# Kernel tuning notes

Hardware: AMD Instinct MI355X
Metric: run time of the kernel (lower is better)

The kernel has to match this reference:

```python
import jax, jax.numpy as jnp
import numpy as np
from jax import lax

B_SZ, C_IN, C_OUT, H_IM, W_IM = 2, 128, 128, 64, 64
N_STATE = 16
DT_RANK = 4  # ceil(128/32)


def _ln_cf(x, w, b, eps=1e-6):
    # channels_first LayerNorm over channel dim
    u = x.mean(1, keepdims=True)
    s = ((x - u) ** 2).mean(1, keepdims=True)
    return w[None, :, None, None] * (x - u) / jnp.sqrt(s + eps) + b[None, :, None, None]


def _bn_train(x, g, b, eps=1e-5):
    # BatchNorm2d in training mode (batch statistics, biased variance)
    m = x.mean((0, 2, 3), keepdims=True)
    v = ((x - m) ** 2).mean((0, 2, 3), keepdims=True)
    return g[None, :, None, None] * (x - m) / jnp.sqrt(v + eps) + b[None, :, None, None]


def _dwconv(x, w, b):
    y = lax.conv_general_dilated(x, w, (1, 1), 'SAME', feature_group_count=x.shape[1],
                                 dimension_numbers=('NCHW', 'OIHW', 'NCHW'))
    return y + b[None, :, None, None]


def _conv1x1(x, w, b):
    return jnp.einsum('oi,bihw->bohw', w, x) + b[None, :, None, None]


def _selective_scan(u, dt, A, Bm, Cm, D, delta_bias):
    # u, dt: [B,Ch,L]; A: [Ch,N]; Bm, Cm: [B,N,L]; D: [Ch]
    dt = jax.nn.softplus(dt + delta_bias[None, :, None])
    xs = (dt.transpose(2, 0, 1), u.transpose(2, 0, 1), Bm.transpose(2, 0, 1), Cm.transpose(2, 0, 1))
    h0 = jnp.zeros(u.shape[:2] + (A.shape[1],), u.dtype)

    def step(h, inp):
        dt_t, u_t, b_t, c_t = inp
        dA = jnp.exp(dt_t[..., None] * A)                        # [B,Ch,N]
        h = h * dA + (dt_t * u_t)[..., None] * b_t[:, None, :]   # [B,Ch,N]
        return h, jnp.einsum('bcn,bn->bc', h, c_t)

    _, ys = lax.scan(step, h0, xs)
    return ys.transpose(1, 2, 0) + u * D[None, :, None]


def _ssm_apply(u, Wx, bx, Wdt, bdt, Alog, D, r):
    # u: [B,Ch,L]. Replicates torch row-major .reshape of [(B L),D] -> [B,D,L].
    Bb, Ch, L = u.shape
    N = Alog.shape[1]
    x_flat = u.transpose(0, 2, 1).reshape(Bb * L, Ch)   # 'b c l -> (b l) c'
    x_dbl = x_flat @ Wx.T + bx
    dt = (x_dbl[:, :r] @ Wdt.T + bdt).reshape(Bb, Wdt.shape[0], L)
    Bm = x_dbl[:, r:r + N].reshape(Bb, N, L)
    Cm = x_dbl[:, r + N:].reshape(Bb, N, L)
    return _selective_scan(u, dt, -jnp.exp(Alog), Bm, Cm, D, bdt)


def _forward(x, ln_in_w, ln_in_b, inproj_w, inproj_b, ln_mamba_w, ln_mamba_b, convm_w, convm_b,
             convr_w, convr_b, ln_cat_w, ln_cat_b, xproj_f_w, xproj_f_b, dtproj_f_w, dtproj_f_b,
             Alog_f, D_f, xproj_b_w, xproj_b_b, dtproj_b_w, dtproj_b_b, Alog_b, D_b,
             xproj_u_w, xproj_u_b, dtproj_u_w, dtproj_u_b, Alog_u, D_u, gate1_w, gate1_b,
             bn_g, bn_b, gate2_w, gate2_b, outproj_w, outproj_b, outln_w, outln_b):
    Bb, C, H, W = x.shape
    L = H * W
    half = C // 2
    x = _ln_cf(x, ln_in_w, ln_in_b)
    xp = _conv1x1(x, inproj_w, inproj_b)
    x_mamba, x_res = xp[:, :C], xp[:, C:]
    x_mamba = _ln_cf(x_mamba, ln_mamba_w, ln_mamba_b)
    x_mamba = jax.nn.silu(_dwconv(x_mamba, convm_w, convm_b))
    x_res = jax.nn.silu(_dwconv(x_res, convr_w, convr_b))
    # forward scan on first half of channels
    xf = x_mamba[:, :half].reshape(Bb, half, L)
    yf = _ssm_apply(xf, xproj_f_w, xproj_f_b, dtproj_f_w, dtproj_f_b, Alog_f, D_f, DT_RANK).reshape(Bb, half, H, W)
    # backward scan on second half (flip H,W, scan, flip back)
    xb = x_mamba[:, half:][:, :, ::-1, ::-1]
    yb = _ssm_apply(xb.reshape(Bb, half, L), xproj_b_w, xproj_b_b, dtproj_b_w, dtproj_b_b,
                    Alog_b, D_b, DT_RANK).reshape(Bb, half, H, W)[:, :, ::-1, ::-1]
    concat = _ln_cf(jnp.concatenate([yf, yb], axis=1), ln_cat_w, ln_cat_b)
    # uncertainty-ordered scan on full x_mamba
    sig = jax.nn.sigmoid(x_mamba.mean(1, keepdims=True))
    unc = (-(sig * jnp.log(sig + 1e-6))).reshape(Bb, L)
    idx = jnp.argsort(-unc, axis=1)       # descending uncertainty
    inv = jnp.argsort(idx, axis=1)        # inverse permutation
    xs = jnp.take_along_axis(x_mamba.reshape(Bb, C, L), idx[:, None, :], axis=2)
    yu = _ssm_apply(xs, xproj_u_w, xproj_u_b, dtproj_u_w, dtproj_u_b, Alog_u, D_u, 2 * DT_RANK)
    yu = jnp.take_along_axis(yu, inv[:, None, :], axis=2).reshape(Bb, C, H, W)
    # gated fusion
    g = jax.nn.relu(_bn_train(_conv1x1(jnp.concatenate([concat, yu], 1), gate1_w, gate1_b), bn_g, bn_b))
    g = jax.nn.sigmoid(_conv1x1(g, gate2_w, gate2_b))
    fused = g * yu + (1.0 - g) * concat
    out = _conv1x1(jnp.concatenate([fused, x_res], 1), outproj_w, outproj_b)
    return _ln_cf(out, outln_w, outln_b)


def setup_inputs() -> dict:
    key = jax.random.key(0)
    ks = jax.random.split(key, 16)
    C, half, R, N = C_IN, C_IN // 2, DT_RANK, N_STATE
    rn = lambda k, shp, s=0.02: jax.random.normal(k, shp, jnp.float32) * s

    def inv_dt(k, n):
        dt = jnp.exp(jax.random.uniform(k, (n,)) * (np.log(0.1) - np.log(0.001)) + np.log(0.001))
        dt = jnp.maximum(dt, 1e-4)
        return dt + jnp.log(-jnp.expm1(-dt))

    std = R ** -0.5
    Alog_h = jnp.log(jnp.broadcast_to(jnp.arange(1, N + 1, dtype=jnp.float32), (half, N)))
    Alog_fl = jnp.log(jnp.broadcast_to(jnp.arange(1, N + 1, dtype=jnp.float32), (C, N)))
    return {
        'x': jax.random.normal(ks[0], (B_SZ, C, H_IM, W_IM), jnp.float32),
        'ln_in_w': jnp.ones(C), 'ln_in_b': jnp.zeros(C),
        'inproj_w': rn(ks[1], (2 * C, C)), 'inproj_b': jnp.zeros(2 * C),
        'ln_mamba_w': jnp.ones(C), 'ln_mamba_b': jnp.zeros(C),
        'convm_w': rn(ks[2], (C, 1, 3, 3), 0.1), 'convm_b': jnp.zeros(C),
        'convr_w': rn(ks[3], (C, 1, 3, 3), 0.1), 'convr_b': jnp.zeros(C),
        'ln_cat_w': jnp.ones(C), 'ln_cat_b': jnp.zeros(C),
        'xproj_f_w': rn(ks[4], (R + 2 * N, half)), 'xproj_f_b': jnp.zeros(R + 2 * N),
        'dtproj_f_w': jax.random.uniform(ks[5], (half, R), minval=-std, maxval=std),
        'dtproj_f_b': inv_dt(ks[6], half),
        'Alog_f': Alog_h, 'D_f': jnp.ones(half),
        'xproj_b_w': rn(ks[7], (R + 2 * N, half)), 'xproj_b_b': jnp.zeros(R + 2 * N),
        'dtproj_b_w': jax.random.uniform(ks[8], (half, R), minval=-std, maxval=std),
        'dtproj_b_b': inv_dt(ks[9], half),
        'Alog_b': Alog_h, 'D_b': jnp.ones(half),
        'xproj_u_w': rn(ks[10], (2 * R + 2 * N, C)), 'xproj_u_b': jnp.zeros(2 * R + 2 * N),
        'dtproj_u_w': jax.random.uniform(ks[11], (C, 2 * R), minval=-std, maxval=std),
        'dtproj_u_b': inv_dt(ks[12], C),
        'Alog_u': Alog_fl, 'D_u': jnp.ones(C),
        'gate1_w': rn(ks[13], (C, 2 * C)), 'gate1_b': jnp.zeros(C),
        'bn_g': jnp.ones(C), 'bn_b': jnp.zeros(C),
        'gate2_w': rn(ks[14], (C, C)), 'gate2_b': jnp.zeros(C),
        'outproj_w': rn(ks[15], (C_OUT, 2 * C)), 'outproj_b': jnp.zeros(C_OUT),
        'outln_w': jnp.ones(C_OUT), 'outln_b': jnp.zeros(C_OUT),
    }


def reference(x, ln_in_w, ln_in_b, inproj_w, inproj_b, ln_mamba_w, ln_mamba_b, convm_w, convm_b,
              convr_w, convr_b, ln_cat_w, ln_cat_b, xproj_f_w, xproj_f_b, dtproj_f_w, dtproj_f_b,
              Alog_f, D_f, xproj_b_w, xproj_b_b, dtproj_b_w, dtproj_b_b, Alog_b, D_b,
              xproj_u_w, xproj_u_b, dtproj_u_w, dtproj_u_b, Alog_u, D_u, gate1_w, gate1_b,
              bn_g, bn_b, gate2_w, gate2_b, outproj_w, outproj_b, outln_w, outln_b):
    return _forward(x, ln_in_w, ln_in_b, inproj_w, inproj_b, ln_mamba_w, ln_mamba_b, convm_w, convm_b,
                    convr_w, convr_b, ln_cat_w, ln_cat_b, xproj_f_w, xproj_f_b, dtproj_f_w, dtproj_f_b,
                    Alog_f, D_f, xproj_b_w, xproj_b_b, dtproj_b_w, dtproj_b_b, Alog_b, D_b,
                    xproj_u_w, xproj_u_b, dtproj_u_w, dtproj_u_b, Alog_u, D_u, gate1_w, gate1_b,
                    bn_g, bn_b, gate2_w, gate2_b, outproj_w, outproj_b, outln_w, outln_b)
```

## Files before the change

kernel.cpp:

```cpp
#include <hip/hip_runtime.h>
#include <cstdint>
#include <cstddef>

#define TPB 256

namespace {

constexpr int B_SZ = 2;
constexpr int C    = 128;
constexpr int HALF = 64;
constexpr int L    = 4096;
constexpr int N    = 16;
constexpr int HH   = 64;
constexpr int WW   = 64;

__device__ __forceinline__ float softplusf(float x) {
  return fmaxf(x, 0.f) + __logf(1.f + __expf(-fabsf(x)));
}
__device__ __forceinline__ float sigm(float x) { return 1.f / (1.f + __expf(-x)); }

__device__ __forceinline__ unsigned long long unc_key(float u, int i) {
  unsigned m = __float_as_uint(u);
  m = (m & 0x80000000u) ? ~m : (m | 0x80000000u);
  return ((unsigned long long)(~m) << 32) | (unsigned)i;
}

__global__ void k_conv_ln(const float* __restrict__ X, int bsX,
                          const float* __restrict__ lnw, const float* __restrict__ lnb,
                          const float* __restrict__ W, const float* __restrict__ bias,
                          float* __restrict__ Y, int I, int O,
                          float* __restrict__ st1s, float* __restrict__ st1q) {
  constexpr int O_PB = 8;
  __shared__ float Wl[O_PB * 128];
  __shared__ float aw[128], ab[128];
  const int o0 = blockIdx.y * O_PB;
  const int b  = blockIdx.z;
  for (int t = threadIdx.x; t < O_PB * I; t += TPB) {
    int i = t / O_PB, k = t % O_PB;
    Wl[t] = W[(size_t)(o0 + k) * I + i];
  }
  for (int t = threadIdx.x; t < I; t += TPB) { aw[t] = lnw[t]; ab[t] = lnb[t]; }
  __syncthreads();
  const int l0 = blockIdx.x * (2 * TPB) + threadIdx.x;
  const int l1 = l0 + TPB;
  const float* X0 = X + (size_t)b * bsX + l0;
  const float* X1 = X + (size_t)b * bsX + l1;
  float s0 = 0.f, q0 = 0.f, s1 = 0.f, q1 = 0.f;
#pragma unroll 8
  for (int i = 0; i < I; ++i) {
    float v0 = X0[(size_t)i * L], v1 = X1[(size_t)i * L];
    s0 += v0; q0 += v0 * v0; s1 += v1; q1 += v1 * v1;
  }
  const float m0 = s0 / I, m1 = s1 / I;
  const float r0 = rsqrtf(q0 / I - m0 * m0 + 1e-6f);
  const float r1 = rsqrtf(q1 / I - m1 * m1 + 1e-6f);
  float acc0[O_PB], acc1[O_PB];
#pragma unroll
  for (int k = 0; k < O_PB; ++k) { acc0[k] = bias[o0 + k]; acc1[k] = acc0[k]; }
#pragma unroll 4
  for (int i = 0; i < I; ++i) {
    float xv0 = (X0[(size_t)i * L] - m0) * r0 * aw[i] + ab[i];
    float xv1 = (X1[(size_t)i * L] - m1) * r1 * aw[i] + ab[i];
#pragma unroll
    for (int k = 0; k < O_PB; ++k) {
      acc0[k] += Wl[i * O_PB + k] * xv0;
      acc1[k] += Wl[i * O_PB + k] * xv1;
    }
  }
#pragma unroll
  for (int k = 0; k < O_PB; ++k) {
    Y[((size_t)b * O + o0 + k) * L + l0] = acc0[k];
    Y[((size_t)b * O + o0 + k) * L + l1] = acc1[k];
  }
  if (o0 < 128) {
    float ss0 = 0.f, qq0 = 0.f, ss1 = 0.f, qq1 = 0.f;
#pragma unroll
    for (int k = 0; k < O_PB; ++k) {
      ss0 += acc0[k]; qq0 += acc0[k] * acc0[k];
      ss1 += acc1[k]; qq1 += acc1[k] * acc1[k];
    }
    atomicAdd(&st1s[b * L + l0], ss0);
    atomicAdd(&st1q[b * L + l0], qq0);
    atomicAdd(&st1s[b * L + l1], ss1);
    atomicAdd(&st1q[b * L + l1], qq1);
  }
}

__global__ void k_dwconv_t(const float* __restrict__ xp,
                           const float* __restrict__ st1s, const float* __restrict__ st1q,
                           const float* __restrict__ lnw, const float* __restrict__ lnb,
                           const float* __restrict__ Wm, const float* __restrict__ bm,
                           const float* __restrict__ Wr, const float* __restrict__ br,
                           float* __restrict__ xm, float* __restrict__ xr) {
  const int c = blockIdx.y;
  const int z = blockIdx.z;
  const int b = z & 1, mode = z >> 1;
  const int h0 = blockIdx.x * 4;
  __shared__ float T[6][66];
  const float* Xc = xp + ((size_t)b * 2 * C + (mode ? C + c : c)) * L;
  const float lw = mode ? 0.f : lnw[c];
  const float lb2 = mode ? 0.f : lnb[c];
  for (int t = threadIdx.x; t < 6 * 66; t += TPB) {
    int r = t / 66, cc = t % 66 - 1;
    int hh = h0 - 1 + r;
    float v = 0.f;
    if (hh >= 0 && hh < HH && cc >= 0 && cc < WW) {
      int li = hh * WW + cc;
      v = Xc[li];
      if (mode == 0) {
        float sv = st1s[b * L + li], qv = st1q[b * L + li];
        float m = sv * (1.f / 128.f);
        float rr = rsqrtf(qv * (1.f / 128.f) - m * m + 1e-6f);
        v = (v - m) * rr * lw + lb2;
      }
    }
    T[r][t % 66] = v;
  }
  __syncthreads();
  const int hl = threadIdx.x >> 6, w = threadIdx.x & 63;
  const float* W9 = (mode ? Wr : Wm) + c * 9;
  float acc = mode ? br[c] : bm[c];
#pragma unroll
  for (int kh = 0; kh < 3; ++kh)
#pragma unroll
    for (int kw = 0; kw < 3; ++kw)
      acc += T[hl + kh][w + kw] * W9[kh * 3 + kw];
  const int l = (h0 + hl) * WW + w;
  float* Yp = mode ? xr : xm;
  Yp[((size_t)b * C + c) * L + l] = acc * sigm(acc);
}

__global__ void k_unc(const float* __restrict__ xm, float* __restrict__ unc) {
  const int lp = threadIdx.x & 63;
  const int wv = threadIdx.x >> 6;
  const int p  = blockIdx.x * 64 + lp;
  const int b = p / L, l = p % L;
  const float* Xp = xm + (size_t)b * C * L + l;
  float s = 0.f;
#pragma unroll 8
  for (int i = 0; i < 32; ++i) s += Xp[(size_t)(wv * 32 + i) * L];
  __shared__ float r1[4][64];
  r1[wv][lp] = s;
  __syncthreads();
  if (wv == 0) {
    float st = r1[0][lp] + r1[1][lp] + r1[2][lp] + r1[3][lp];
    float sg = sigm(st / C);
    unc[p] = -(sg * __logf(sg + 1e-6f));
  }
}

__global__ void k_rank(const float* __restrict__ unc, int* __restrict__ rankbuf) {
  constexpr int JC = 512;
  __shared__ unsigned long long K[JC];
  const int b  = blockIdx.z;
  const int j0 = blockIdx.y * JC;
  const int i  = blockIdx.x * TPB + threadIdx.x;
  for (int t = threadIdx.x; t < JC; t += TPB)
    K[t] = unc_key(unc[b * L + j0 + t], j0 + t);
  __syncthreads();
  const unsigned long long my = unc_key(unc[b * L + i], i);
  int cnt = 0;
#pragma unroll 8
  for (int j = 0; j < JC; ++j) cnt += (K[j] < my) ? 1 : 0;
  atomicAdd(&rankbuf[b * L + i], cnt);
}

__global__ void k_scatgath(const float* __restrict__ xm, const int* __restrict__ rankbuf,
                           float* __restrict__ xs, int* __restrict__ inv,
                           int* __restrict__ idx) {
  int t = blockIdx.x * TPB + threadIdx.x;
  int l = t % L, c = (t / L) % C, b = t / (C * L);
  int r = rankbuf[b * L + l];
  xs[((size_t)b * C + c) * L + r] = xm[t];
  if (c == 0) { inv[b * L + l] = r; idx[b * L + r] = l; }
}

__global__ void k_convx_all(const float* __restrict__ xm, const float* __restrict__ xs,
                            const float* __restrict__ Wf, const float* __restrict__ bf,
                            const float* __restrict__ Wb, const float* __restrict__ bb,
                            const float* __restrict__ Wu, const float* __restrict__ bu,
                            float* __restrict__ XDF, float* __restrict__ XDU) {
  const int z = blockIdx.z;
  const bool isU = z >= 4;
  const int I = isU ? 128 : 64;
  const int O = isU ? 40 : 36;
  const int o0 = blockIdx.y * 4;
  if (o0 >= O) return;
  int b, dir;
  const float *W, *bi;
  if (!isU) { dir = z >> 1; b = z & 1; W = dir ? Wb : Wf; bi = dir ? bb : bf; }
  else      { dir = 0; b = z - 4; W = Wu; bi = bu; }
  __shared__ float Wl[4 * 128];
  for (int t = threadIdx.x; t < 4 * I; t += TPB) {
    int i = t / 4, k = t % 4;
    Wl[t] = W[(size_t)(o0 + k) * I + i];
  }
  __syncthreads();
  const int l = blockIdx.x * TPB + threadIdx.x;
  const int ls = isU ? l : (dir ? (L - 1 - l) : l);
  const float* Xb = isU ? (xs + (size_t)b * C * L)
                        : (xm + ((size_t)b * C + dir * HALF) * L);
  float acc[4];
#pragma unroll
  for (int k = 0; k < 4; ++k) acc[k] = bi[o0 + k];
#pragma unroll 4
  for (int i = 0; i < I; ++i) {
    float xv = Xb[(size_t)i * L + ls];
#pragma unroll
    for (int k = 0; k < 4; ++k) acc[k] += Wl[i * 4 + k] * xv;
  }
  float* yp = isU ? (XDU + ((size_t)b * L + l) * 40 + o0)
                  : (XDF + ((size_t)z * L + l) * 36 + o0);
#pragma unroll
  for (int k = 0; k < 4; ++k) yp[k] = acc[k];
}

__global__ void k_bc_all(const float* __restrict__ xdblF, const float* __restrict__ xdblU,
                         float* __restrict__ BmTF, float* __restrict__ CmTF,
                         float* __restrict__ BmTU, float* __restrict__ CmTU) {
  const int z = blockIdx.z;
  const bool isU = z >= 4;
  const int RT = isU ? 8 : 4, OT = isU ? 40 : 36;
  const float* src = isU ? (xdblU + (size_t)(z - 4) * L * 40)
                         : (xdblF + (size_t)z * L * 36);
  float* BT = isU ? (BmTU + (size_t)(z - 4) * L * N) : (BmTF + (size_t)z * L * N);
  float* CT = isU ? (CmTU + (size_t)(z - 4) * L * N) : (CmTF + (size_t)z * L * N);
  const int n = blockIdx.y;
  const int l2 = blockIdx.x * TPB + threadIdx.x;
  int f2 = n * L + l2;
  int lb = f2 >> 4, cb = f2 & 15;
  const float* xr2 = src + (size_t)lb * OT + RT + cb;
  size_t ob = (size_t)l2 * N + n;
  BT[ob] = xr2[0];
  CT[ob] = xr2[N];
}

__global__ __launch_bounds__(1024) void
k_scan_all(const float* __restrict__ xdblF, const float* __restrict__ xdblU,
           const float* __restrict__ dtf_w, const float* __restrict__ dtf_b,
           const float* __restrict__ dtb_w, const float* __restrict__ dtb_b,
           const float* __restrict__ dtu_w, const float* __restrict__ dtu_b,
           const float* __restrict__ xm, const float* __restrict__ xs,
           const int* __restrict__ idx,
           const float* __restrict__ BmTF, const float* __restrict__ CmTF,
           const float* __restrict__ BmTU, const float* __restrict__ CmTU,
           const float* __restrict__ Alog_f, const float* __restrict__ Alog_b,
           const float* __restrict__ Alog_u,
           const float* __restrict__ D_f, const float* __restrict__ D_b,
           const float* __restrict__ D_u,
           float* __restrict__ yf, float* __restrict__ yb, float* __restrict__ yu) {
  const int blk = blockIdx.x;
  const int tid = threadIdx.x;
  const bool isU = blk >= 256;
  int CsT, RT, c, b, dir;
  const float *Wdt, *bdt, *Alog, *Dv, *xdbl, *BT, *CT, *Ub;
  const int* idxb = nullptr;
  float* Y;
  int OT;
  if (!isU) {
    CsT = 64; RT = 4; OT = 36;
    int zb = blk >> 6; c = blk & 63; dir = zb >> 1; b = zb & 1;
    Wdt = dir ? dtb_w : dtf_w; bdt = dir ? dtb_b : dtf_b;
    Alog = dir ? Alog_b : Alog_f; Dv = dir ? D_b : D_f;
    xdbl = xdblF + (size_t)zb * L * 36;
    BT = BmTF + (size_t)zb * L * N; CT = CmTF + (size_t)zb * L * N;
    Ub = xm + ((size_t)b * C + dir * HALF + c) * L;
    Y = (dir ? yb : yf) + ((size_t)b * HALF + c) * L;
  } else {
    CsT = 128; RT = 8; OT = 40;
    int blk2 = blk - 256; b = blk2 >> 7; c = blk2 & 127; dir = 0;
    Wdt = dtu_w; bdt = dtu_b; Alog = Alog_u; Dv = D_u;
    xdbl = xdblU + (size_t)b * L * 40;
    BT = BmTU + (size_t)b * L * N; CT = CmTU + (size_t)b * L * N;
    Ub = xs + ((size_t)b * C + c) * L;
    idxb = idx + b * L;
    Y = yu + ((size_t)b * C + c) * L;
  }
  __shared__ float sW[1024];
  __shared__ float sb2[128];
  __shared__ float dtL[64][65];
  __shared__ float uL[64][65];
  __shared__ float sA[N][65], sH[N][65];
  for (int t = tid; t < CsT * RT; t += 1024) {
    int csrc = t / RT, r = t % RT;
    sW[r * CsT + csrc] = Wdt[t];
  }
  for (int t = tid; t < CsT; t += 1024) sb2[t] = bdt[t];
  __syncthreads();
  {
    const int chunk_d = tid >> 4;
    const int sq = (tid & 15) * 4;
    const int lsrc = isU ? (c * 32 + (chunk_d >> 1)) : (c * 64 + chunk_d);
    const float* xrp = xdbl + (size_t)lsrc * OT;
    float xr[8];
    for (int r = 0; r < RT; ++r) xr[r] = xrp[r];
    const float bcc = sb2[c];
#pragma unroll
    for (int j = 0; j < 4; ++j) {
      int s = sq + j;
      int csrc = isU ? (((chunk_d & 1) << 6) + s) : s;
      float acc = sb2[csrc] + bcc;
      for (int r = 0; r < RT; ++r) acc += sW[r * CsT + csrc] * xr[r];
      int l = (chunk_d << 6) + s;
      dtL[chunk_d][s] = softplusf(acc);
      uL[chunk_d][s] = Ub[isU ? l : (dir ? (L - 1 - l) : l)];
    }
  }
  __syncthreads();
  const int n = tid & 15;
  const int chunk = tid >> 4;
  const float a = -__expf(Alog[c * N + n]);
  const float* bp = BT + ((size_t)(chunk << 6)) * N + n;
  const float* cp = CT + ((size_t)(chunk << 6)) * N + n;
  float ap = 1.f, h = 0.f;
#pragma unroll 4
  for (int s = 0; s < 64; ++s) {
    float d = dtL[chunk][s];
    float uv = uL[chunk][s];
    float bn = bp[(size_t)s * N];
    float dA = __expf(d * a);
    ap *= dA;
    h = h * dA + d * uv * bn;
  }
  sA[n][chunk] = ap; sH[n][chunk] = h;
  __syncthreads();
  {
    const int w = tid >> 6;
    const int k = tid & 63;
    float A = sA[w][k];
    float Bv = sH[w][k];
#pragma unroll
    for (int j = 1; j < 64; j <<= 1) {
      float pa = __shfl_up(A, j);
      float pb = __shfl_up(Bv, j);
      if (k >= j) { Bv = pb * A + Bv; A = pa * A; }
    }
    float hprev = __shfl_up(Bv, 1);
    sH[w][k] = (k == 0) ? 0.f : hprev;
  }
  __syncthreads();
  h = sH[n][chunk];
  const float Dc = Dv[c];
  float ybuf[4];
#pragma unroll 4
  for (int s = 0; s < 64; ++s) {
    float d = dtL[chunk][s];
    float uv = uL[chunk][s];
    float bn = bp[(size_t)s * N];
    float cn = cp[(size_t)s * N];
    float dA = __expf(d * a);
    h = h * dA + d * uv * bn;
    float p = h * cn;
    p += __shfl_xor(p, 1);
    p += __shfl_xor(p, 2);
    p += __shfl_xor(p, 4);
    p += __shfl_xor(p, 8);
    if ((s & 15) == n) ybuf[s >> 4] = p + uv * Dc;
  }
  if (!isU) {
    float* Yp = Y + (chunk << 6);
#pragma unroll
    for (int q = 0; q < 4; ++q) Yp[16 * q + n] = ybuf[q];
  } else {
    const int s0 = chunk << 6;
#pragma unroll
    for (int q = 0; q < 4; ++q) Y[idxb[s0 + 16 * q + n]] = ybuf[q];
  }
}

template <int O_PB>
__global__ void k_gate1(const float* __restrict__ yf, const float* __restrict__ yb,
                        const float* __restrict__ lncw, const float* __restrict__ lncb,
                        const float* __restrict__ yu,
                        const float* __restrict__ W, const float* __restrict__ bias,
                        float* __restrict__ g1,
                        float* __restrict__ st2m, float* __restrict__ st2r,
                        float* __restrict__ bnsum) {
  __shared__ float Wl[O_PB * 256];
  __shared__ float cw[128], cb2[128];
  __shared__ float part[2][O_PB][4];
  const int o0 = blockIdx.y * O_PB;
  const int b  = blockIdx.z;
  for (int t = threadIdx.x; t < O_PB * 256; t += TPB) {
    int i = t / O_PB, k = t % O_PB;
    Wl[t] = W[(size_t)(o0 + k) * 256 + i];
  }
  for (int t = threadIdx.x; t < 128; t += TPB) { cw[t] = lncw[t]; cb2[t] = lncb[t]; }
  __syncthreads();
  const int l = blockIdx.x * TPB + threadIdx.x;
  const float* f0 = yf + (size_t)b * HALF * L + l;
  const float* b0 = yb + (size_t)b * HALF * L + (L - 1 - l);
  const float* u0 = yu + (size_t)b * C * L + l;
  float s = 0.f, s2 = 0.f;
#pragma unroll 8
  for (int i = 0; i < 64; ++i) { float v = f0[(size_t)i * L]; s += v; s2 += v * v; }
#pragma unroll 8
  for (int i = 0; i < 64; ++i) { float v = b0[(size_t)i * L]; s += v; s2 += v * v; }
  const float m = s / C;
  const float r = rsqrtf(s2 / C - m * m + 1e-6f);
  if (blockIdx.y == 0) { st2m[b * L + l] = m; st2r[b * L + l] = r; }
  float acc[O_PB];
#pragma unroll
  for (int k = 0; k < O_PB; ++k) acc[k] = bias[o0 + k];
#pragma unroll 4
  for (int i = 0; i < 64; ++i) {
    float cv = (f0[(size_t)i * L] - m) * r * cw[i] + cb2[i];
#pragma unroll
    for (int k = 0; k < O_PB; ++k) acc[k] += Wl[i * O_PB + k] * cv;
  }
#pragma unroll 4
  for (int i = 0; i < 64; ++i) {
    float cv = (b0[(size_t)i * L] - m) * r * cw[64 + i] + cb2[64 + i];
#pragma unroll
    for (int k = 0; k < O_PB; ++k) acc[k] += Wl[(64 + i) * O_PB + k] * cv;
  }
#pragma unroll 4
  for (int i = 0; i < 128; ++i) {
    float xv = u0[(size_t)i * L];
#pragma unroll
    for (int k = 0; k < O_PB; ++k) acc[k] += Wl[(128 + i) * O_PB + k] * xv;
  }
#pragma unroll
  for (int k = 0; k < O_PB; ++k)
    g1[((size_t)b * C + o0 + k) * L + l] = acc[k];
  const int wv = threadIdx.x >> 6, lnn = threadIdx.x & 63;
#pragma unroll
  for (int k = 0; k < O_PB; ++k) {
    float v = acc[k];
    v += __shfl_xor(v, 1);  v += __shfl_xor(v, 2);  v += __shfl_xor(v, 4);
    v += __shfl_xor(v, 8);  v += __shfl_xor(v, 16); v += __shfl_xor(v, 32);
    if (lnn == 0) part[0][k][wv] = v;
    float q = acc[k] * acc[k];
    q += __shfl_xor(q, 1);  q += __shfl_xor(q, 2);  q += __shfl_xor(q, 4);
    q += __shfl_xor(q, 8);  q += __shfl_xor(q, 16); q += __shfl_xor(q, 32);
    if (lnn == 0) part[1][k][wv] = q;
  }
  __syncthreads();
  if (threadIdx.x < 2 * O_PB) {
    int which = threadIdx.x >= O_PB, k = threadIdx.x % O_PB;
    float v = part[which][k][0] + part[which][k][1] + part[which][k][2] + part[which][k][3];
    atomicAdd(&bnsum[which * 128 + o0 + k], v);
  }
}

template <int O_PB>
__global__ void k_gate2_fuse(const float* __restrict__ g1,
                             const float* __restrict__ bnsum,
                             const float* __restrict__ bn_g, const float* __restrict__ bn_b,
                             const float* __restrict__ W, const float* __restrict__ bias,
                             const float* __restrict__ yu,
                             const float* __restrict__ yf, const float* __restrict__ yb,
                             const float* __restrict__ mean2, const float* __restrict__ rinv2,
                             const float* __restrict__ lncw, const float* __restrict__ lncb,
                             float* __restrict__ fused) {
  __shared__ float Wl[O_PB * 128];
  __shared__ float sc[128], sh[128];
  __shared__ float cwo[O_PB], cbo[O_PB];
  const int o0 = blockIdx.y * O_PB;
  const int b  = blockIdx.z;
  for (int t = threadIdx.x; t < O_PB * 128; t += TPB) {
    int i = t / O_PB, k = t % O_PB;
    Wl[t] = W[(size_t)(o0 + k) * 128 + i];
  }
  for (int t = threadIdx.x; t < 128; t += TPB) {
    float sv = bnsum[t], qv = bnsum[128 + t];
    float mean = sv / (B_SZ * L);
    float var  = qv / (B_SZ * L) - mean * mean;
    float scv = bn_g[t] * rsqrtf(var + 1e-5f);
    sc[t] = scv;
    sh[t] = bn_b[t] - mean * scv;
  }
  if (threadIdx.x < O_PB) {
    cwo[threadIdx.x] = lncw[o0 + threadIdx.x];
    cbo[threadIdx.x] = lncb[o0 + threadIdx.x];
  }
  __syncthreads();
  const int l = blockIdx.x * TPB + threadIdx.x;
  const float m = mean2[b * L + l], r = rinv2[b * L + l];
  const float* Xb = g1 + (size_t)b * C * L + l;
  float acc[O_PB];
#pragma unroll
  for (int k = 0; k < O_PB; ++k) acc[k] = bias[o0 + k];
#pragma unroll 4
  for (int i = 0; i < 128; ++i) {
    float v = fmaxf(Xb[(size_t)i * L] * sc[i] + sh[i], 0.f);
#pragma unroll
    for (int k = 0; k < O_PB; ++k) acc[k] += Wl[i * O_PB + k] * v;
  }
#pragma unroll
  for (int k = 0; k < O_PB; ++k) {
    int o = o0 + k;
    float g = sigm(acc[k]);
    float yuv = yu[((size_t)b * C + o) * L + l];
    float yv = (o < 64) ? yf[((size_t)b * HALF + o) * L + l]
                        : yb[((size_t)b * HALF + (o - 64)) * L + (L - 1 - l)];
    float cv = (yv - m) * r * cwo[k] + cbo[k];
    fused[((size_t)b * C + o) * L + l] = g * yuv + (1.f - g) * cv;
  }
}

template <int O_PB>
__global__ void k_conv1x1_cat2(const float* __restrict__ X1, const float* __restrict__ X2,
                               const float* __restrict__ W, const float* __restrict__ bias,
                               float* __restrict__ Y, int O) {
  __shared__ float Wl[O_PB * 256];
  const int o0 = blockIdx.y * O_PB;
  const int b  = blockIdx.z;
  for (int t = threadIdx.x; t < O_PB * 256; t += TPB) {
    int i = t / O_PB, k = t % O_PB;
    Wl[t] = W[(size_t)(o0 + k) * 256 + i];
  }
  __syncthreads();
  const int l = blockIdx.x * TPB + threadIdx.x;
  const float* Xb1 = X1 + (size_t)b * C * L + l;
  const float* Xb2 = X2 + (size_t)b * C * L + l;
  float acc[O_PB];
#pragma unroll
  for (int k = 0; k < O_PB; ++k) acc[k] = bias[o0 + k];
#pragma unroll 4
  for (int i = 0; i < 128; ++i) {
    float xv = Xb1[(size_t)i * L];
#pragma unroll
    for (int k = 0; k < O_PB; ++k) acc[k] += Wl[i * O_PB + k] * xv;
  }
#pragma unroll 4
  for (int i = 0; i < 128; ++i) {
    float xv = Xb2[(size_t)i * L];
#pragma unroll
    for (int k = 0; k < O_PB; ++k) acc[k] += Wl[(128 + i) * O_PB + k] * xv;
  }
#pragma unroll
  for (int k = 0; k < O_PB; ++k)
    Y[((size_t)b * O + o0 + k) * L + l] = acc[k];
}

__global__ void k_ln_cf(const float* __restrict__ X,
                        const float* __restrict__ w, const float* __restrict__ bchan,
                        float* __restrict__ Y) {
  const int lp = threadIdx.x & 63;
  const int wv = threadIdx.x >> 6;
  const int p  = blockIdx.x * 64 + lp;
  const int b = p / L, l = p % L;
  const float* Xp = X + (size_t)b * C * L + l;
  float s = 0.f, s2 = 0.f;
#pragma unroll 8
  for (int i = 0; i < 32; ++i) {
    float v = Xp[(size_t)(wv * 32 + i) * L];
    s += v; s2 += v * v;
  }
  __shared__ float r1[4][64], r2[4][64];
  r1[wv][lp] = s; r2[wv][lp] = s2;
  __syncthreads();
  float st  = r1[0][lp] + r1[1][lp] + r1[2][lp] + r1[3][lp];
  float s2t = r2[0][lp] + r2[1][lp] + r2[2][lp] + r2[3][lp];
  float mean = st / C;
  float rinv = rsqrtf(s2t / C - mean * mean + 1e-6f);
  float* Yp = Y + (size_t)b * C * L + l;
#pragma unroll 8
  for (int i = 0; i < 32; ++i) {
    int c = wv * 32 + i;
    float v = Xp[(size_t)c * L];
    Yp[(size_t)c * L] = w[c] * (v - mean) * rinv + bchan[c];
  }
}

}

extern "C" void kernel_launch(void* const* d_in, const int* in_sizes, int n_in,
                              void* d_out, int out_size, void* d_ws, size_t ws_size,
                              hipStream_t stream) {
  const float* x         = (const float*)d_in[0];
  const float* ln_in_w   = (const float*)d_in[1];
  const float* ln_in_b   = (const float*)d_in[2];
  const float* inproj_w  = (const float*)d_in[3];
  const float* inproj_b  = (const float*)d_in[4];
  const float* ln_m_w    = (const float*)d_in[5];
  const float* ln_m_b    = (const float*)d_in[6];
  const float* convm_w   = (const float*)d_in[7];
  const float* convm_b   = (const float*)d_in[8];
  const float* convr_w   = (const float*)d_in[9];
  const float* convr_b   = (const float*)d_in[10];
  const float* ln_cat_w  = (const float*)d_in[11];
  const float* ln_cat_b  = (const float*)d_in[12];
  const float* xpf_w     = (const float*)d_in[13];
  const float* xpf_b     = (const float*)d_in[14];
  const float* dtf_w     = (const float*)d_in[15];
  const float* dtf_b     = (const float*)d_in[16];
  const float* Alog_f    = (const float*)d_in[17];
  const float* D_f       = (const float*)d_in[18];
  const float* xpb_w     = (const float*)d_in[19];
  const float* xpb_b     = (const float*)d_in[20];
  const float* dtb_w     = (const float*)d_in[21];
  const float* dtb_b     = (const float*)d_in[22];
  const float* Alog_b    = (const float*)d_in[23];
  const float* D_b       = (const float*)d_in[24];
  const float* xpu_w     = (const float*)d_in[25];
  const float* xpu_b     = (const float*)d_in[26];
  const float* dtu_w     = (const float*)d_in[27];
  const float* dtu_b     = (const float*)d_in[28];
  const float* Alog_u    = (const float*)d_in[29];
  const float* D_u       = (const float*)d_in[30];
  const float* gate1_w   = (const float*)d_in[31];
  const float* gate1_b   = (const float*)d_in[32];
  const float* bn_g      = (const float*)d_in[33];
  const float* bn_b      = (const float*)d_in[34];
  const float* gate2_w   = (const float*)d_in[35];
  const float* gate2_b   = (const float*)d_in[36];
  const float* outproj_w = (const float*)d_in[37];
  const float* outproj_b = (const float*)d_in[38];
  const float* outln_w   = (const float*)d_in[39];
  const float* outln_b   = (const float*)d_in[40];

  float* ws = (float*)d_ws;
  size_t off = 0;
  auto alloc = [&](size_t n) { float* p = ws + off; off += n; return p; };

  const size_t BL = (size_t)B_SZ * L;
  float* st1s  = alloc(BL);
  float* st1q  = alloc(BL);
  int*   rank  = (int*)alloc(BL);
  float* bnsum = alloc(256);
  const size_t zeroBytes = (3 * BL + 256) * sizeof(float);

  float* xp    = alloc((size_t)B_SZ * 2 * C * L);
  float* xm    = alloc((size_t)B_SZ * C * L);
  float* xr    = alloc((size_t)B_SZ * C * L);
  float* unc   = alloc(BL);
  int*   inv   = (int*)alloc(BL);
  int*   idx   = (int*)alloc(BL);
  float* xs    = alloc((size_t)B_SZ * C * L);
  float* xdblF = alloc((size_t)4 * L * 36);
  float* BmTF  = alloc((size_t)4 * L * N);
  float* CmTF  = alloc((size_t)4 * L * N);
  float* xdblU = alloc((size_t)2 * L * 40);
  float* BmTU  = alloc((size_t)2 * L * N);
  float* CmTU  = alloc((size_t)2 * L * N);
  float* yf    = alloc((size_t)B_SZ * HALF * L);
  float* yb    = alloc((size_t)B_SZ * HALF * L);
  float* yu    = alloc((size_t)B_SZ * C * L);
  float* st2m  = alloc(BL);
  float* st2r  = alloc(BL);
  float* g1    = alloc((size_t)B_SZ * C * L);
  float* fused = alloc((size_t)B_SZ * C * L);
  float* outp  = alloc((size_t)B_SZ * C * L);
  (void)ws_size; (void)in_sizes; (void)n_in; (void)out_size;

  const int pixB = B_SZ * L / 64;
  const int elemB = B_SZ * C * L / TPB;

  hipMemsetAsync(st1s, 0, zeroBytes, stream);
  k_conv_ln<<<dim3(L / (2 * TPB), 32, B_SZ), TPB, 0, stream>>>(
      x, C * L, ln_in_w, ln_in_b, inproj_w, inproj_b, xp, 128, 256, st1s, st1q);
  k_dwconv_t<<<dim3(HH / 4, C, 2 * B_SZ), TPB, 0, stream>>>(
      xp, st1s, st1q, ln_m_w, ln_m_b, convm_w, convm_b, convr_w, convr_b, xm, xr);
  k_unc<<<pixB, TPB, 0, stream>>>(xm, unc);
  k_rank<<<dim3(L / TPB, 8, B_SZ), TPB, 0, stream>>>(unc, rank);
  k_scatgath<<<elemB, TPB, 0, stream>>>(xm, rank, xs, inv, idx);
  k_convx_all<<<dim3(L / TPB, 10, 6), TPB, 0, stream>>>(
      xm, xs, xpf_w, xpf_b, xpb_w, xpb_b, xpu_w, xpu_b, xdblF, xdblU);
  k_bc_all<<<dim3(L / TPB, N, 6), TPB, 0, stream>>>(
      xdblF, xdblU, BmTF, CmTF, BmTU, CmTU);
  k_scan_all<<<512, 1024, 0, stream>>>(
      xdblF, xdblU, dtf_w, dtf_b, dtb_w, dtb_b, dtu_w, dtu_b,
      xm, xs, idx, BmTF, CmTF, BmTU, CmTU,
      Alog_f, Alog_b, Alog_u, D_f, D_b, D_u, yf, yb, yu);
  k_gate1<8><<<dim3(L / TPB, 16, B_SZ), TPB, 0, stream>>>(
      yf, yb, ln_cat_w, ln_cat_b, yu, gate1_w, gate1_b, g1, st2m, st2r, bnsum);
  k_gate2_fuse<8><<<dim3(L / TPB, 16, B_SZ), TPB, 0, stream>>>(
      g1, bnsum, bn_g, bn_b, gate2_w, gate2_b, yu, yf, yb, st2m, st2r,
      ln_cat_w, ln_cat_b, fused);
  k_conv1x1_cat2<8><<<dim3(L / TPB, 16, B_SZ), TPB, 0, stream>>>(
      fused, xr, outproj_w, outproj_b, outp, 128);
  k_ln_cf<<<pixB, TPB, 0, stream>>>(outp, outln_w, outln_b, (float*)d_out);
}
```

Measured before the change: 341.8 us.

## Fuse B/C transpose into scan via vectorized xdbl reads; cache LN inputs in registers

Removes the k_bc_all kernel and its BmT/CmT scratch buffers. The scan now reads the B and C rows straight from xdbl with float4 loads, using the row-major reshape mapping (n<<8 + chunk<<2 + sb). The input conv+LN kernel now processes one pixel per thread and keeps all 128 channel values in registers, so x is not read from global memory twice. The price is higher register pressure (a 128-float array) and float4 loads whose alignment depends on the row strides of 36 and 40.

```diff
diff --git a/kernel.cpp b/kernel.cpp
--- a/kernel.cpp
+++ b/kernel.cpp
@@ -28,9 +28,10 @@
 __global__ void k_conv_ln(const float* __restrict__ X, int bsX,
                           const float* __restrict__ lnw, const float* __restrict__ lnb,
                           const float* __restrict__ W, const float* __restrict__ bias,
-                          float* __restrict__ Y, int I, int O,
+                          float* __restrict__ Y, int O,
                           float* __restrict__ st1s, float* __restrict__ st1q) {
   constexpr int O_PB = 8;
+  constexpr int I = 128;
   __shared__ float Wl[O_PB * 128];
   __shared__ float aw[128], ab[128];
   const int o0 = blockIdx.y * O_PB;
@@ -41,48 +42,35 @@
   }
   for (int t = threadIdx.x; t < I; t += TPB) { aw[t] = lnw[t]; ab[t] = lnb[t]; }
   __syncthreads();
-  const int l0 = blockIdx.x * (2 * TPB) + threadIdx.x;
-  const int l1 = l0 + TPB;
-  const float* X0 = X + (size_t)b * bsX + l0;
-  const float* X1 = X + (size_t)b * bsX + l1;
-  float s0 = 0.f, q0 = 0.f, s1 = 0.f, q1 = 0.f;
-#pragma unroll 8
+  const int l = blockIdx.x * TPB + threadIdx.x;
+  const float* X0 = X + (size_t)b * bsX + l;
+  float xv[I];
+  float s = 0.f, q = 0.f;
+#pragma unroll
   for (int i = 0; i < I; ++i) {
-    float v0 = X0[(size_t)i * L], v1 = X1[(size_t)i * L];
-    s0 += v0; q0 += v0 * v0; s1 += v1; q1 += v1 * v1;
-  }
-  const float m0 = s0 / I, m1 = s1 / I;
-  const float r0 = rsqrtf(q0 / I - m0 * m0 + 1e-6f);
-  const float r1 = rsqrtf(q1 / I - m1 * m1 + 1e-6f);
-  float acc0[O_PB], acc1[O_PB];
-#pragma unroll
-  for (int k = 0; k < O_PB; ++k) { acc0[k] = bias[o0 + k]; acc1[k] = acc0[k]; }
-#pragma unroll 4
+    float v = X0[(size_t)i * L];
+    xv[i] = v; s += v; q += v * v;
+  }
+  const float m = s * (1.f / I);
+  const float r = rsqrtf(q * (1.f / I) - m * m + 1e-6f);
+  float acc[O_PB];
+#pragma unroll
+  for (int k = 0; k < O_PB; ++k) acc[k] = bias[o0 + k];
+#pragma unroll
   for (int i = 0; i < I; ++i) {
-    float xv0 = (X0[(size_t)i * L] - m0) * r0 * aw[i] + ab[i];
-    float xv1 = (X1[(size_t)i * L] - m1) * r1 * aw[i] + ab[i];
-#pragma unroll
-    for (int k = 0; k < O_PB; ++k) {
-      acc0[k] += Wl[i * O_PB + k] * xv0;
-      acc1[k] += Wl[i * O_PB + k] * xv1;
-    }
-  }
-#pragma unroll
-  for (int k = 0; k < O_PB; ++k) {
-    Y[((size_t)b * O + o0 + k) * L + l0] = acc0[k];
-    Y[((size_t)b * O + o0 + k) * L + l1] = acc1[k];
-  }
+    float t = (xv[i] - m) * r * aw[i] + ab[i];
+#pragma unroll
+    for (int k = 0; k < O_PB; ++k) acc[k] += Wl[i * O_PB + k] * t;
+  }
+#pragma unroll
+  for (int k = 0; k < O_PB; ++k)
+    Y[((size_t)b * O + o0 + k) * L + l] = acc[k];
   if (o0 < 128) {
-    float ss0 = 0.f, qq0 = 0.f, ss1 = 0.f, qq1 = 0.f;
-#pragma unroll
-    for (int k = 0; k < O_PB; ++k) {
-      ss0 += acc0[k]; qq0 += acc0[k] * acc0[k];
-      ss1 += acc1[k]; qq1 += acc1[k] * acc1[k];
-    }
-    atomicAdd(&st1s[b * L + l0], ss0);
-    atomicAdd(&st1q[b * L + l0], qq0);
-    atomicAdd(&st1s[b * L + l1], ss1);
-    atomicAdd(&st1q[b * L + l1], qq1);
+    float ss = 0.f, qq = 0.f;
+#pragma unroll
+    for (int k = 0; k < O_PB; ++k) { ss += acc[k]; qq += acc[k] * acc[k]; }
+    atomicAdd(&st1s[b * L + l], ss);
+    atomicAdd(&st1q[b * L + l], qq);
   }
 }
 
@@ -215,26 +203,6 @@
   for (int k = 0; k < 4; ++k) yp[k] = acc[k];
 }
 
-__global__ void k_bc_all(const float* __restrict__ xdblF, const float* __restrict__ xdblU,
-                         float* __restrict__ BmTF, float* __restrict__ CmTF,
-                         float* __restrict__ BmTU, float* __restrict__ CmTU) {
-  const int z = blockIdx.z;
-  const bool isU = z >= 4;
-  const int RT = isU ? 8 : 4, OT = isU ? 40 : 36;
-  const float* src = isU ? (xdblU + (size_t)(z - 4) * L * 40)
-                         : (xdblF + (size_t)z * L * 36);
-  float* BT = isU ? (BmTU + (size_t)(z - 4) * L * N) : (BmTF + (size_t)z * L * N);
-  float* CT = isU ? (CmTU + (size_t)(z - 4) * L * N) : (CmTF + (size_t)z * L * N);
-  const int n = blockIdx.y;
-  const int l2 = blockIdx.x * TPB + threadIdx.x;
-  int f2 = n * L + l2;
-  int lb = f2 >> 4, cb = f2 & 15;
-  const float* xr2 = src + (size_t)lb * OT + RT + cb;
-  size_t ob = (size_t)l2 * N + n;
-  BT[ob] = xr2[0];
-  CT[ob] = xr2[N];
-}
-
 __global__ __launch_bounds__(1024) void
 k_scan_all(const float* __restrict__ xdblF, const float* __restrict__ xdblU,
            const float* __restrict__ dtf_w, const float* __restrict__ dtf_b,
@@ -242,8 +210,6 @@
            const float* __restrict__ dtu_w, const float* __restrict__ dtu_b,
            const float* __restrict__ xm, const float* __restrict__ xs,
            const int* __restrict__ idx,
-           const float* __restrict__ BmTF, const float* __restrict__ CmTF,
-           const float* __restrict__ BmTU, const float* __restrict__ CmTU,
            const float* __restrict__ Alog_f, const float* __restrict__ Alog_b,
            const float* __restrict__ Alog_u,
            const float* __restrict__ D_f, const float* __restrict__ D_b,
@@ -253,7 +219,7 @@
   const int tid = threadIdx.x;
   const bool isU = blk >= 256;
   int CsT, RT, c, b, dir;
-  const float *Wdt, *bdt, *Alog, *Dv, *xdbl, *BT, *CT, *Ub;
+  const float *Wdt, *bdt, *Alog, *Dv, *xdbl, *Ub;
   const int* idxb = nullptr;
   float* Y;
   int OT;
@@ -263,7 +229,6 @@
     Wdt = dir ? dtb_w : dtf_w; bdt = dir ? dtb_b : dtf_b;
     Alog = dir ? Alog_b : Alog_f; Dv = dir ? D_b : D_f;
     xdbl = xdblF + (size_t)zb * L * 36;
-    BT = BmTF + (size_t)zb * L * N; CT = CmTF + (size_t)zb * L * N;
     Ub = xm + ((size_t)b * C + dir * HALF + c) * L;
     Y = (dir ? yb : yf) + ((size_t)b * HALF + c) * L;
   } else {
@@ -271,7 +236,6 @@
     int blk2 = blk - 256; b = blk2 >> 7; c = blk2 & 127; dir = 0;
     Wdt = dtu_w; bdt = dtu_b; Alog = Alog_u; Dv = D_u;
     xdbl = xdblU + (size_t)b * L * 40;
-    BT = BmTU + (size_t)b * L * N; CT = CmTU + (size_t)b * L * N;
     Ub = xs + ((size_t)b * C + c) * L;
     idxb = idx + b * L;
     Y = yu + ((size_t)b * C + c) * L;
@@ -310,17 +274,25 @@
   const int n = tid & 15;
   const int chunk = tid >> 4;
   const float a = -__expf(Alog[c * N + n]);
-  const float* bp = BT + ((size_t)(chunk << 6)) * N + n;
-  const float* cp = CT + ((size_t)(chunk << 6)) * N + n;
   float ap = 1.f, h = 0.f;
-#pragma unroll 4
-  for (int s = 0; s < 64; ++s) {
-    float d = dtL[chunk][s];
-    float uv = uL[chunk][s];
-    float bn = bp[(size_t)s * N];
-    float dA = __expf(d * a);
-    ap *= dA;
-    h = h * dA + d * uv * bn;
+#pragma unroll
+  for (int sb = 0; sb < 4; ++sb) {
+    const float* rp = xdbl + (size_t)((n << 8) + (chunk << 2) + sb) * OT + RT;
+    float4 q0 = *(const float4*)rp;
+    float4 q1 = *(const float4*)(rp + 4);
+    float4 q2 = *(const float4*)(rp + 8);
+    float4 q3 = *(const float4*)(rp + 12);
+    float bv[16] = {q0.x, q0.y, q0.z, q0.w, q1.x, q1.y, q1.z, q1.w,
+                    q2.x, q2.y, q2.z, q2.w, q3.x, q3.y, q3.z, q3.w};
+#pragma unroll
+    for (int j = 0; j < 16; ++j) {
+      int s = (sb << 4) + j;
+      float d = dtL[chunk][s];
+      float uv = uL[chunk][s];
+      float dA = __expf(d * a);
+      ap *= dA;
+      h = h * dA + d * uv * bv[j];
+    }
   }
   sA[n][chunk] = ap; sH[n][chunk] = h;
   __syncthreads();
@@ -342,20 +314,35 @@
   h = sH[n][chunk];
   const float Dc = Dv[c];
   float ybuf[4];
-#pragma unroll 4
-  for (int s = 0; s < 64; ++s) {
-    float d = dtL[chunk][s];
-    float uv = uL[chunk][s];
-    float bn = bp[(size_t)s * N];
-    float cn = cp[(size_t)s * N];
-    float dA = __expf(d * a);
-    h = h * dA + d * uv * bn;
-    float p = h * cn;
-    p += __shfl_xor(p, 1);
-    p += __shfl_xor(p, 2);
-    p += __shfl_xor(p, 4);
-    p += __shfl_xor(p, 8);
-    if ((s & 15) == n) ybuf[s >> 4] = p + uv * Dc;
+#pragma unroll
+  for (int sb = 0; sb < 4; ++sb) {
+    const float* rp = xdbl + (size_t)((n << 8) + (chunk << 2) + sb) * OT + RT;
+    float4 q0 = *(const float4*)rp;
+    float4 q1 = *(const float4*)(rp + 4);
+    float4 q2 = *(const float4*)(rp + 8);
+    float4 q3 = *(const float4*)(rp + 12);
+    float4 r0 = *(const float4*)(rp + 16);
+    float4 r1 = *(const float4*)(rp + 20);
+    float4 r2 = *(const float4*)(rp + 24);
+    float4 r3 = *(const float4*)(rp + 28);
+    float bv[16] = {q0.x, q0.y, q0.z, q0.w, q1.x, q1.y, q1.z, q1.w,
+                    q2.x, q2.y, q2.z, q2.w, q3.x, q3.y, q3.z, q3.w};
+    float cv[16] = {r0.x, r0.y, r0.z, r0.w, r1.x, r1.y, r1.z, r1.w,
+                    r2.x, r2.y, r2.z, r2.w, r3.x, r3.y, r3.z, r3.w};
+#pragma unroll
+    for (int j = 0; j < 16; ++j) {
+      int s = (sb << 4) + j;
+      float d = dtL[chunk][s];
+      float uv = uL[chunk][s];
+      float dA = __expf(d * a);
+      h = h * dA + d * uv * bv[j];
+      float p = h * cv[j];
+      p += __shfl_xor(p, 1);
+      p += __shfl_xor(p, 2);
+      p += __shfl_xor(p, 4);
+      p += __shfl_xor(p, 8);
+      if (j == n) ybuf[sb] = p + uv * Dc;
+    }
   }
   if (!isU) {
     float* Yp = Y + (chunk << 6);
@@ -630,11 +617,7 @@
   int*   idx   = (int*)alloc(BL);
   float* xs    = alloc((size_t)B_SZ * C * L);
   float* xdblF = alloc((size_t)4 * L * 36);
-  float* BmTF  = alloc((size_t)4 * L * N);
-  float* CmTF  = alloc((size_t)4 * L * N);
   float* xdblU = alloc((size_t)2 * L * 40);
-  float* BmTU  = alloc((size_t)2 * L * N);
-  float* CmTU  = alloc((size_t)2 * L * N);
   float* yf    = alloc((size_t)B_SZ * HALF * L);
   float* yb    = alloc((size_t)B_SZ * HALF * L);
   float* yu    = alloc((size_t)B_SZ * C * L);
@@ -649,8 +632,8 @@
   const int elemB = B_SZ * C * L / TPB;
 
   hipMemsetAsync(st1s, 0, zeroBytes, stream);
-  k_conv_ln<<<dim3(L / (2 * TPB), 32, B_SZ), TPB, 0, stream>>>(
-      x, C * L, ln_in_w, ln_in_b, inproj_w, inproj_b, xp, 128, 256, st1s, st1q);
+  k_conv_ln<<<dim3(L / TPB, 32, B_SZ), TPB, 0, stream>>>(
+      x, C * L, ln_in_w, ln_in_b, inproj_w, inproj_b, xp, 256, st1s, st1q);
   k_dwconv_t<<<dim3(HH / 4, C, 2 * B_SZ), TPB, 0, stream>>>(
       xp, st1s, st1q, ln_m_w, ln_m_b, convm_w, convm_b, convr_w, convr_b, xm, xr);
   k_unc<<<pixB, TPB, 0, stream>>>(xm, unc);
@@ -658,12 +641,9 @@
   k_scatgath<<<elemB, TPB, 0, stream>>>(xm, rank, xs, inv, idx);
   k_convx_all<<<dim3(L / TPB, 10, 6), TPB, 0, stream>>>(
       xm, xs, xpf_w, xpf_b, xpb_w, xpb_b, xpu_w, xpu_b, xdblF, xdblU);
-  k_bc_all<<<dim3(L / TPB, N, 6), TPB, 0, stream>>>(
-      xdblF, xdblU, BmTF, CmTF, BmTU, CmTU);
   k_scan_all<<<512, 1024, 0, stream>>>(
       xdblF, xdblU, dtf_w, dtf_b, dtb_w, dtb_b, dtu_w, dtu_b,
-      xm, xs, idx, BmTF, CmTF, BmTU, CmTU,
-      Alog_f, Alog_b, Alog_u, D_f, D_b, D_u, yf, yb, yu);
+      xm, xs, idx, Alog_f, Alog_b, Alog_u, D_f, D_b, D_u, yf, yb, yu);
   k_gate1<8><<<dim3(L / TPB, 16, B_SZ), TPB, 0, stream>>>(
       yf, yb, ln_cat_w, ln_cat_b, yu, gate1_w, gate1_b, g1, st2m, st2r, bnsum);
   k_gate2_fuse<8><<<dim3(L / TPB, 16, B_SZ), TPB, 0, stream>>>(
```

New measurement: 496.9 us. +45.4%, slower.
